# Optimization experiments

Hardware: AMD Instinct MI355X
Metric: run time of the kernel (lower is better)

The kernel has to match this reference:

```python
import jax, jax.numpy as jnp
import numpy as np

B, S, HID = 1, 2048, 1024
H, HKV, D = 16, 4, 64
THETA = 10000.0


def _rope_tables(seq_len, head_dim):
    # Matches RotaryEmbedding: emb = cat(freqs, freqs); kernel reads cos/sin at even
    # positions d for each rotated pair (d, d+1), i.e. columns 0::2 of the table.
    inv_freq = 1.0 / (THETA ** (jnp.arange(0, head_dim, 2, dtype=jnp.float32) / head_dim))
    freqs = jnp.arange(seq_len, dtype=jnp.float32)[:, None] * inv_freq[None, :]  # [S, D/2]
    emb = jnp.concatenate([freqs, freqs], axis=-1)  # [S, D]
    return jnp.cos(emb)[:, 0::2], jnp.sin(emb)[:, 0::2]  # each [S, D/2]


def _apply_rope(x, cos, sin):
    # x: [B, H, S, D]; rotate interleaved pairs (2i, 2i+1) as in the kernel.
    xe, xo = x[..., 0::2], x[..., 1::2]
    re = xe * cos - xo * sin
    ro = xe * sin + xo * cos
    return jnp.stack([re, ro], axis=-1).reshape(x.shape)


def setup_inputs() -> dict:
    key = jax.random.key(0)
    k0, k1, k2, k3, k4 = jax.random.split(key, 5)
    return {
        "hidden_states": jax.random.normal(k0, (B, S, HID), dtype=jnp.float32),
        "Wq": jax.random.normal(k1, (HID, H * D), dtype=jnp.float32) * 0.02,
        "Wk": jax.random.normal(k2, (HID, HKV * D), dtype=jnp.float32) * 0.02,
        "Wv": jax.random.normal(k3, (HID, HKV * D), dtype=jnp.float32) * 0.02,
        "Wo": jax.random.normal(k4, (H * D, HID), dtype=jnp.float32) * 0.02,
    }


def reference(hidden_states, Wq, Wk, Wv, Wo):
    b, s, _ = hidden_states.shape
    q = (hidden_states @ Wq).reshape(b, s, H, D).transpose(0, 2, 1, 3)    # [B,H,S,D]
    k = (hidden_states @ Wk).reshape(b, s, HKV, D).transpose(0, 2, 1, 3)  # [B,Hkv,S,D]
    v = (hidden_states @ Wv).reshape(b, s, HKV, D).transpose(0, 2, 1, 3)

    cos, sin = _rope_tables(s, D)
    q = _apply_rope(q, cos, sin)
    k = _apply_rope(k, cos, sin)

    G = H // HKV  # GQA group size: query head h -> kv head h // G
    qg = q.reshape(b, HKV, G, s, D)
    scale = jnp.float32(D) ** -0.5
    scores = jnp.einsum("bkgqd,bkpd->bkgqp", qg, k) * scale  # [B,Hkv,G,S,S]
    causal = jnp.tril(jnp.ones((s, s), dtype=bool))
    scores = jnp.where(causal, scores, jnp.float32(-1e30))
    probs = jax.nn.softmax(scores, axis=-1)
    out = jnp.einsum("bkgqp,bkpd->bkgqd", probs, v).reshape(b, H, s, D)
    out = out.transpose(0, 2, 1, 3).reshape(b, s, H * D)
    return out @ Wo
```

## Files before the change

kernel.cpp:

```cpp
#include <hip/hip_runtime.h>
#include <hip/hip_bf16.h>
#include <math.h>

#define SEQ   2048
#define HID   1024
#define NH    16
#define NKV   4
#define DH    64
#define GQ    (NH / NKV)
#define NQKV  1536
#define KT    64
#define QB    32
#define CH    512
#define NCH   (SEQ / CH)
#define PSTR  72
#define LNSC  0.2878231366f
#define GS    528
#define BUFS  (8 * GS)

typedef __attribute__((ext_vector_type(8))) short bf16x8;
typedef __attribute__((ext_vector_type(4))) float f32x4;
typedef unsigned short u16;
typedef unsigned int u32;

__device__ __forceinline__ u16 f2bf(float f) {
    union { float f; unsigned u; } x; x.f = f;
    unsigned r = x.u + 0x7fffu + ((x.u >> 16) & 1u);
    return (u16)(r >> 16);
}
__device__ __forceinline__ u32 pk2bf(float lo, float hi) {
    return (u32)f2bf(lo) | ((u32)f2bf(hi) << 16);
}
__device__ __forceinline__ void load_lds16(const u16* g, u16* l) {
    __builtin_amdgcn_global_load_lds(
        (const __attribute__((address_space(1))) unsigned int*)g,
        (__attribute__((address_space(3))) unsigned int*)l, 16, 0, 0);
}

__global__ __launch_bounds__(256) void setup(const float* __restrict__ X,
                                             const float* __restrict__ Wq,
                                             const float* __restrict__ Wk,
                                             const float* __restrict__ Wv,
                                             const float* __restrict__ Wo,
                                             u16* __restrict__ Xb,
                                             u16* __restrict__ Wt,
                                             u16* __restrict__ WoT) {
    const int z = blockIdx.z;
    if (z == 4) {
        const int idx = ((int)blockIdx.y * 64 + (int)blockIdx.x) * 256 + threadIdx.x;
        const float4 v = ((const float4*)X)[idx];
        ushort4 o;
        o.x = f2bf(v.x); o.y = f2bf(v.y); o.z = f2bf(v.z); o.w = f2bf(v.w);
        ((ushort4*)Xb)[idx] = o;
        return;
    }
    const float* in; u16* out; int N;
    if (z == 0)      { in = Wq; out = Wt;                             N = HID; }
    else if (z == 1) { in = Wk; out = Wt + (size_t)HID * HID;         N = 256; }
    else if (z == 2) { in = Wv; out = Wt + (size_t)(HID + 256) * HID; N = 256; }
    else             { in = Wo; out = WoT;                            N = HID; }

    const int n0 = blockIdx.x * 32;
    if (n0 >= N) return;
    const int k0 = blockIdx.y * 32;

    __shared__ float t[32][33];
    const int tx = threadIdx.x & 31;
    const int ty = threadIdx.x >> 5;
    #pragma unroll
    for (int i = 0; i < 4; ++i)
        t[ty + i * 8][tx] = in[(size_t)(k0 + ty + i * 8) * N + n0 + tx];
    __syncthreads();
    #pragma unroll
    for (int i = 0; i < 4; ++i)
        out[(size_t)(n0 + ty + i * 8) * HID + k0 + tx] = f2bf(t[tx][ty + i * 8]);
}

__global__ __launch_bounds__(256) void gemm_qkv(const u16* __restrict__ A,
                                                const u16* __restrict__ Bt,
                                                u16* __restrict__ Qb,
                                                u16* __restrict__ Kb,
                                                u16* __restrict__ VTg) {
    __shared__ u16 Bs[2 * BUFS];

    const int tid  = threadIdx.x;
    const int lane = tid & 63;
    const int w    = tid >> 6;
    const int c    = lane & 15;
    const int quad = lane >> 4;
    const int m0   = blockIdx.y * 64;
    const int n0   = blockIdx.x * 64;

    const u16* gB0 = Bt + (size_t)(n0 + w * 16 + (lane >> 3)) * HID + (lane & 7) * 8;
    const u16* gB1 = gB0 + (size_t)8 * HID;
    const int  gofs0 = (w * 2) * GS, gofs1 = (w * 2 + 1) * GS;

    const u16* gA = A + (size_t)(m0 + w * 16 + c) * HID + quad * 8;
    const int  bfoff = (c >> 3) * GS + (c & 7) * 64 + quad * 8;

    f32x4 acc[4];
    #pragma unroll
    for (int nt = 0; nt < 4; ++nt) acc[nt] = (f32x4){0.f, 0.f, 0.f, 0.f};

    bf16x8 afc[2], afn[2];
    afc[0] = *(const bf16x8*)gA;
    afc[1] = *(const bf16x8*)(gA + 32);
    load_lds16(gB0, &Bs[gofs0]);
    load_lds16(gB1, &Bs[gofs1]);

    const int T = HID / 64;
    for (int t = 0; t < T; ++t) {
        __syncthreads();
        if (t + 1 < T) {
            const int nb = ((t + 1) & 1) * BUFS;
            load_lds16(gB0 + (t + 1) * 64, &Bs[nb + gofs0]);
            load_lds16(gB1 + (t + 1) * 64, &Bs[nb + gofs1]);
            afn[0] = *(const bf16x8*)(gA + (t + 1) * 64);
            afn[1] = *(const bf16x8*)(gA + (t + 1) * 64 + 32);
        }
        const int b = (t & 1) * BUFS;
        bf16x8 bfr[4][2];
        #pragma unroll
        for (int nt = 0; nt < 4; ++nt)
            #pragma unroll
            for (int ks = 0; ks < 2; ++ks)
                bfr[nt][ks] = *(const bf16x8*)&Bs[b + nt * (2 * GS) + ks * 32 + bfoff];
        #pragma unroll
        for (int ks = 0; ks < 2; ++ks)
            #pragma unroll
            for (int nt = 0; nt < 4; ++nt)
                acc[nt] = __builtin_amdgcn_mfma_f32_16x16x32_bf16(afc[ks], bfr[nt][ks], acc[nt], 0, 0, 0);
        afc[0] = afn[0];
        afc[1] = afn[1];
    }

    const int s0 = m0 + w * 16 + quad * 4;
    if (n0 < 1280) {
        const bool isQ = (n0 < 1024);
        #pragma unroll
        for (int nt = 0; nt < 4; ++nt) {
            const int d = nt * 16 + c;
            const float inv_freq = __expf(-(float)(d & 30) * LNSC);
            const float sgn = (d & 1) ? 1.f : -1.f;
            #pragma unroll
            for (int rg = 0; rg < 4; ++rg) {
                const float self = acc[nt][rg];
                const float partner = __shfl_xor(self, 1);
                float sn, cs;
                __sincosf((float)(s0 + rg) * inv_freq, &sn, &cs);
                float o = fmaf(partner, sgn * sn, self * cs);
                if (isQ) {
                    Qb[(size_t)(s0 + rg) * HID + n0 + d] = f2bf(o * 0.125f);
                } else {
                    const int kh = (n0 - 1024) >> 6;
                    Kb[((size_t)kh * SEQ + s0 + rg) * DH + d] = f2bf(o);
                }
            }
        }
    } else {
        const int kh = (n0 - 1280) >> 6;
        #pragma unroll
        for (int nt = 0; nt < 4; ++nt) {
            const int d = nt * 16 + c;
            ushort4 o;
            o.x = f2bf(acc[nt][0]); o.y = f2bf(acc[nt][1]);
            o.z = f2bf(acc[nt][2]); o.w = f2bf(acc[nt][3]);
            *(ushort4*)&VTg[((size_t)kh * DH + d) * SEQ + s0] = o;
        }
    }
}

__global__ __launch_bounds__(256) void gemm64(const u16* __restrict__ A,
                                              const u16* __restrict__ Bt,
                                              float* __restrict__ C,
                                              int K, int ldc) {
    __shared__ u16 Bs[2 * BUFS];

    const int tid  = threadIdx.x;
    const int lane = tid & 63;
    const int w    = tid >> 6;
    const int c    = lane & 15;
    const int quad = lane >> 4;
    const int m0   = blockIdx.y * 64;
    const int n0   = blockIdx.x * 64;

    const u16* gB0 = Bt + (size_t)(n0 + w * 16 + (lane >> 3)) * K + (lane & 7) * 8;
    const u16* gB1 = gB0 + (size_t)8 * K;
    const int  gofs0 = (w * 2) * GS, gofs1 = (w * 2 + 1) * GS;

    const u16* gA = A + (size_t)(m0 + w * 16 + c) * K + quad * 8;
    const int  bfoff = (c >> 3) * GS + (c & 7) * 64 + quad * 8;

    f32x4 acc[4];
    #pragma unroll
    for (int nt = 0; nt < 4; ++nt) acc[nt] = (f32x4){0.f, 0.f, 0.f, 0.f};

    bf16x8 afc[2], afn[2];
    afc[0] = *(const bf16x8*)gA;
    afc[1] = *(const bf16x8*)(gA + 32);
    load_lds16(gB0, &Bs[gofs0]);
    load_lds16(gB1, &Bs[gofs1]);

    const int T = K / 64;
    for (int t = 0; t < T; ++t) {
        __syncthreads();
        if (t + 1 < T) {
            const int nb = ((t + 1) & 1) * BUFS;
            load_lds16(gB0 + (t + 1) * 64, &Bs[nb + gofs0]);
            load_lds16(gB1 + (t + 1) * 64, &Bs[nb + gofs1]);
            afn[0] = *(const bf16x8*)(gA + (t + 1) * 64);
            afn[1] = *(const bf16x8*)(gA + (t + 1) * 64 + 32);
        }
        const int b = (t & 1) * BUFS;
        bf16x8 bfr[4][2];
        #pragma unroll
        for (int nt = 0; nt < 4; ++nt)
            #pragma unroll
            for (int ks = 0; ks < 2; ++ks)
                bfr[nt][ks] = *(const bf16x8*)&Bs[b + nt * (2 * GS) + ks * 32 + bfoff];
        #pragma unroll
        for (int ks = 0; ks < 2; ++ks)
            #pragma unroll
            for (int nt = 0; nt < 4; ++nt)
                acc[nt] = __builtin_amdgcn_mfma_f32_16x16x32_bf16(afc[ks], bfr[nt][ks], acc[nt], 0, 0, 0);
        afc[0] = afn[0];
        afc[1] = afn[1];
    }

    #pragma unroll
    for (int nt = 0; nt < 4; ++nt)
        #pragma unroll
        for (int rg = 0; rg < 4; ++rg)
            C[(size_t)(m0 + w * 16 + quad * 4 + rg) * ldc + n0 + nt * 16 + c] = acc[nt][rg];
}

__global__ __launch_bounds__(256) void attn_kernel(const u16* __restrict__ Qb,
                                                   const u16* __restrict__ Kb,
                                                   const u16* __restrict__ VTg,
                                                   float* __restrict__ Opart,
                                                   float* __restrict__ lpart,
                                                   u16* __restrict__ At) {
    __shared__ u16 Ks[2][2][64 * 32];
    __shared__ u16 Vs[2][2][64 * 32];
    __shared__ u16 Pst[4][QB * PSTR];

    const int tid  = threadIdx.x;
    const int lane = tid & 63;
    const int w    = tid >> 6;
    const int c    = lane & 15;
    const int quad = lane >> 4;
    const int kh   = blockIdx.y;
    const int z    = blockIdx.z;
    const int qt   = (SEQ / QB - 1) - (int)blockIdx.x;
    const int q0   = qt * QB;
    const int h    = kh * GQ + w;

    const int kstart = z * CH;
    const int klim   = q0 + QB;
    if (kstart >= klim) return;
    const int kend   = (klim < kstart + CH) ? klim : (kstart + CH);
    const int ntiles = (kend - kstart + KT - 1) / KT;

    bf16x8 qf[2][2];
    #pragma unroll
    for (int g = 0; g < 2; ++g)
        #pragma unroll
        for (int ks = 0; ks < 2; ++ks)
            qf[g][ks] = *(const bf16x8*)&Qb[(size_t)(q0 + g * 16 + c) * HID + h * DH + ks * 32 + quad * 8];

    f32x4 accO[4][2];
    #pragma unroll
    for (int nt = 0; nt < 4; ++nt)
        #pragma unroll
        for (int g = 0; g < 2; ++g)
            accO[nt][g] = (f32x4){0.f, 0.f, 0.f, 0.f};
    float l[2] = {0.f, 0.f};

    const int hf = w >> 1;
    const int g0 = (w & 1) * 2;
    const int srow = (lane >> 2);
    const int scol = (lane & 3) * 8;

    {
        #pragma unroll
        for (int gi = 0; gi < 2; ++gi) {
            const int g = g0 + gi;
            load_lds16(Kb + ((size_t)kh * SEQ + kstart + g * 16 + srow) * DH + hf * 32 + scol,
                       &Ks[0][hf][(g * 16) * 32]);
            load_lds16(VTg + ((size_t)kh * DH + g * 16 + srow) * SEQ + kstart + hf * 32 + scol,
                       &Vs[0][hf][(g * 16) * 32]);
        }
    }

    for (int t = 0; t < ntiles; ++t) {
        const int kt0 = kstart + t * KT;
        __syncthreads();
        if (t + 1 < ntiles) {
            const int nk = kt0 + KT;
            const int nb = (t + 1) & 1;
            #pragma unroll
            for (int gi = 0; gi < 2; ++gi) {
                const int g = g0 + gi;
                load_lds16(Kb + ((size_t)kh * SEQ + nk + g * 16 + srow) * DH + hf * 32 + scol,
                           &Ks[nb][hf][(g * 16) * 32]);
                load_lds16(VTg + ((size_t)kh * DH + g * 16 + srow) * SEQ + nk + hf * 32 + scol,
                           &Vs[nb][hf][(g * 16) * 32]);
            }
        }
        const int b = t & 1;

        f32x4 accS[4][2];
        #pragma unroll
        for (int nS = 0; nS < 4; ++nS)
            #pragma unroll
            for (int g = 0; g < 2; ++g)
                accS[nS][g] = (f32x4){0.f, 0.f, 0.f, 0.f};
        #pragma unroll
        for (int nS = 0; nS < 4; ++nS)
            #pragma unroll
            for (int ks = 0; ks < 2; ++ks) {
                const bf16x8 kf = *(const bf16x8*)&Ks[b][ks][(nS * 16 + c) * 32 + quad * 8];
                #pragma unroll
                for (int g = 0; g < 2; ++g)
                    accS[nS][g] = __builtin_amdgcn_mfma_f32_16x16x32_bf16(kf, qf[g][ks], accS[nS][g], 0, 0, 0);
            }

        #pragma unroll
        for (int g = 0; g < 2; ++g) {
            const int q = q0 + g * 16 + c;
            #pragma unroll
            for (int nS = 0; nS < 4; ++nS) {
                const int key = kt0 + nS * 16 + quad * 4;
                const float p0 = (key + 0 <= q) ? __expf(accS[nS][g][0]) : 0.f;
                const float p1 = (key + 1 <= q) ? __expf(accS[nS][g][1]) : 0.f;
                const float p2 = (key + 2 <= q) ? __expf(accS[nS][g][2]) : 0.f;
                const float p3 = (key + 3 <= q) ? __expf(accS[nS][g][3]) : 0.f;
                l[g] += (p0 + p1) + (p2 + p3);
                u32* dst = (u32*)&Pst[w][(g * 16 + c) * PSTR + nS * 16 + quad * 4];
                dst[0] = pk2bf(p0, p1);
                dst[1] = pk2bf(p2, p3);
            }
        }
        __threadfence_block();

        #pragma unroll
        for (int ks2 = 0; ks2 < 2; ++ks2) {
            bf16x8 pf[2];
            #pragma unroll
            for (int g = 0; g < 2; ++g)
                pf[g] = *(const bf16x8*)&Pst[w][(g * 16 + c) * PSTR + ks2 * 32 + quad * 8];
            #pragma unroll
            for (int nt = 0; nt < 4; ++nt) {
                const bf16x8 vf = *(const bf16x8*)&Vs[b][ks2][(nt * 16 + c) * 32 + quad * 8];
                #pragma unroll
                for (int g = 0; g < 2; ++g)
                    accO[nt][g] = __builtin_amdgcn_mfma_f32_16x16x32_bf16(vf, pf[g], accO[nt][g], 0, 0, 0);
            }
        }
    }

    const int nchunks = (q0 + QB + CH - 1) / CH;

    if (nchunks == 1) {
        #pragma unroll
        for (int g = 0; g < 2; ++g) {
            float lg = l[g];
            lg += __shfl_xor(lg, 16);
            lg += __shfl_xor(lg, 32);
            const float inv = 1.0f / lg;
            u16* Ap = At + (size_t)(q0 + g * 16 + c) * HID + h * DH;
            #pragma unroll
            for (int nt = 0; nt < 4; ++nt) {
                ushort4 o;
                o.x = f2bf(accO[nt][g][0] * inv);
                o.y = f2bf(accO[nt][g][1] * inv);
                o.z = f2bf(accO[nt][g][2] * inv);
                o.w = f2bf(accO[nt][g][3] * inv);
                *(ushort4*)&Ap[nt * 16 + quad * 4] = o;
            }
        }
        return;
    }

    #pragma unroll
    for (int g = 0; g < 2; ++g) {
        float lg = l[g];
        lg += __shfl_xor(lg, 16);
        lg += __shfl_xor(lg, 32);
        if (quad == 0)
            lpart[((size_t)z * SEQ + q0 + g * 16 + c) * NH + h] = lg;

        float* Op = Opart + ((size_t)z * SEQ + q0 + g * 16 + c) * HID + h * DH;
        #pragma unroll
        for (int nt = 0; nt < 4; ++nt)
            *(f32x4*)&Op[nt * 16 + quad * 4] = accO[nt][g];
    }
}

__global__ __launch_bounds__(256) void attn_reduce(const float* __restrict__ Opart,
                                                   const float* __restrict__ lpart,
                                                   u16* __restrict__ At) {
    const int idx = blockIdx.x * 256 + threadIdx.x + (CH * HID / 4);
    const int q  = idx >> 8;
    const int h  = (idx & 255) >> 4;
    const int klim = (q & ~(QB - 1)) + QB;
    float4 o = ((const float4*)Opart)[idx];
    float  l = lpart[q * NH + h];
    #pragma unroll
    for (int z = 1; z < NCH; ++z) {
        if (z * CH < klim) {
            const float4 o1 = ((const float4*)Opart)[idx + z * (SEQ * HID / 4)];
            o.x += o1.x; o.y += o1.y; o.z += o1.z; o.w += o1.w;
            l += lpart[(z * SEQ + q) * NH + h];
        }
    }
    const float inv = 1.0f / l;
    ushort4 r;
    r.x = f2bf(o.x * inv); r.y = f2bf(o.y * inv);
    r.z = f2bf(o.z * inv); r.w = f2bf(o.w * inv);
    ((ushort4*)At)[idx] = r;
}

extern "C" void kernel_launch(void* const* d_in, const int* in_sizes, int n_in,
                              void* d_out, int out_size, void* d_ws, size_t ws_size,
                              hipStream_t stream) {
    const float* X  = (const float*)d_in[0];
    const float* Wq = (const float*)d_in[1];
    const float* Wk = (const float*)d_in[2];
    const float* Wv = (const float*)d_in[3];
    const float* Wo = (const float*)d_in[4];
    float* out = (float*)d_out;

    u16* Wt     = (u16*)d_ws;
    u16* WoT    = Wt + (size_t)NQKV * HID;
    u16* Xb     = WoT + (size_t)HID * HID;
    u16* At     = Xb + (size_t)SEQ * HID;
    u16* Qb     = At + (size_t)SEQ * HID;
    u16* Kb     = Qb + (size_t)SEQ * HID;
    u16* VTg    = Kb + (size_t)NKV * SEQ * DH;
    float* Opart = (float*)(VTg + (size_t)NKV * DH * SEQ);
    float* lpart = Opart + (size_t)NCH * SEQ * HID;

    dim3 blk(256);

    setup<<<dim3(64, 32, 5), blk, 0, stream>>>(X, Wq, Wk, Wv, Wo, Xb, Wt, WoT);

    gemm_qkv<<<dim3(NQKV / 64, SEQ / 64), blk, 0, stream>>>(Xb, Wt, Qb, Kb, VTg);

    attn_kernel<<<dim3(SEQ / QB, NKV, NCH), blk, 0, stream>>>(Qb, Kb, VTg, Opart, lpart, At);

    attn_reduce<<<((SEQ - CH) * HID / 4) / 256, blk, 0, stream>>>(Opart, lpart, At);

    gemm64<<<dim3(HID / 64, SEQ / 64), blk, 0, stream>>>(At, WoT, out, HID, HID);
}
```

Before: 136.4 us.

## Swizzle K/V LDS tiles, use exp2 with folded log2e, skip masking on full tiles

K and V tiles move from a split half-column LDS layout to full 64-wide rows with an XOR swizzle, applied both to the global-to-LDS load addresses and to the MFMA fragment reads, to avoid bank conflicts. The Q scale now folds in log2(e), so the softmax uses the hardware exp2 instruction instead of __expf. Tiles that lie fully below the causal diagonal skip the per-element mask compares. The software bf16 rounding is replaced by the packed v_cvt_pk_bf16_f32 instruction, whose rounding may differ slightly.

```diff
diff --git a/kernel.cpp b/kernel.cpp
--- a/kernel.cpp
+++ b/kernel.cpp
@@ -17,6 +17,7 @@
 #define LNSC  0.2878231366f
 #define GS    528
 #define BUFS  (8 * GS)
+#define QSCALE 0.18033688011112042f
 
 typedef __attribute__((ext_vector_type(8))) short bf16x8;
 typedef __attribute__((ext_vector_type(4))) float f32x4;
@@ -28,8 +29,10 @@
     unsigned r = x.u + 0x7fffu + ((x.u >> 16) & 1u);
     return (u16)(r >> 16);
 }
-__device__ __forceinline__ u32 pk2bf(float lo, float hi) {
-    return (u32)f2bf(lo) | ((u32)f2bf(hi) << 16);
+__device__ __forceinline__ u32 cvtpk(float lo, float hi) {
+    u32 r;
+    asm("v_cvt_pk_bf16_f32 %0, %1, %2" : "=v"(r) : "v"(lo), "v"(hi));
+    return r;
 }
 __device__ __forceinline__ void load_lds16(const u16* g, u16* l) {
     __builtin_amdgcn_global_load_lds(
@@ -150,7 +153,7 @@
                 __sincosf((float)(s0 + rg) * inv_freq, &sn, &cs);
                 float o = fmaf(partner, sgn * sn, self * cs);
                 if (isQ) {
-                    Qb[(size_t)(s0 + rg) * HID + n0 + d] = f2bf(o * 0.125f);
+                    Qb[(size_t)(s0 + rg) * HID + n0 + d] = f2bf(o * QSCALE);
                 } else {
                     const int kh = (n0 - 1024) >> 6;
                     Kb[((size_t)kh * SEQ + s0 + rg) * DH + d] = f2bf(o);
@@ -240,8 +243,8 @@
                                                    float* __restrict__ Opart,
                                                    float* __restrict__ lpart,
                                                    u16* __restrict__ At) {
-    __shared__ u16 Ks[2][2][64 * 32];
-    __shared__ u16 Vs[2][2][64 * 32];
+    __shared__ u16 Ks[2][64 * 64];
+    __shared__ u16 Vs[2][64 * 64];
     __shared__ u16 Pst[4][QB * PSTR];
 
     const int tid  = threadIdx.x;
@@ -276,20 +279,16 @@
             accO[nt][g] = (f32x4){0.f, 0.f, 0.f, 0.f};
     float l[2] = {0.f, 0.f};
 
-    const int hf = w >> 1;
-    const int g0 = (w & 1) * 2;
-    const int srow = (lane >> 2);
-    const int scol = (lane & 3) * 8;
-
-    {
-        #pragma unroll
-        for (int gi = 0; gi < 2; ++gi) {
-            const int g = g0 + gi;
-            load_lds16(Kb + ((size_t)kh * SEQ + kstart + g * 16 + srow) * DH + hf * 32 + scol,
-                       &Ks[0][hf][(g * 16) * 32]);
-            load_lds16(VTg + ((size_t)kh * DH + g * 16 + srow) * SEQ + kstart + hf * 32 + scol,
-                       &Vs[0][hf][(g * 16) * 32]);
-        }
+    const int rr = lane >> 3;
+    const int sw = ((lane & 7) ^ rr) * 8;
+
+    #pragma unroll
+    for (int gi = 0; gi < 2; ++gi) {
+        const int row = w * 16 + gi * 8;
+        load_lds16(Kb + ((size_t)kh * SEQ + kstart + row + rr) * DH + sw,
+                   &Ks[0][row * 64]);
+        load_lds16(VTg + ((size_t)kh * DH + row + rr) * SEQ + kstart + sw,
+                   &Vs[0][row * 64]);
     }
 
     for (int t = 0; t < ntiles; ++t) {
@@ -300,11 +299,11 @@
             const int nb = (t + 1) & 1;
             #pragma unroll
             for (int gi = 0; gi < 2; ++gi) {
-                const int g = g0 + gi;
-                load_lds16(Kb + ((size_t)kh * SEQ + nk + g * 16 + srow) * DH + hf * 32 + scol,
-                           &Ks[nb][hf][(g * 16) * 32]);
-                load_lds16(VTg + ((size_t)kh * DH + g * 16 + srow) * SEQ + nk + hf * 32 + scol,
-                           &Vs[nb][hf][(g * 16) * 32]);
+                const int row = w * 16 + gi * 8;
+                load_lds16(Kb + ((size_t)kh * SEQ + nk + row + rr) * DH + sw,
+                           &Ks[nb][row * 64]);
+                load_lds16(VTg + ((size_t)kh * DH + row + rr) * SEQ + nk + sw,
+                           &Vs[nb][row * 64]);
             }
         }
         const int b = t & 1;
@@ -319,7 +318,8 @@
         for (int nS = 0; nS < 4; ++nS)
             #pragma unroll
             for (int ks = 0; ks < 2; ++ks) {
-                const bf16x8 kf = *(const bf16x8*)&Ks[b][ks][(nS * 16 + c) * 32 + quad * 8];
+                const bf16x8 kf = *(const bf16x8*)
+                    &Ks[b][(nS * 16 + c) * 64 + (((ks * 4 + quad) ^ (c & 7)) * 8)];
                 #pragma unroll
                 for (int g = 0; g < 2; ++g)
                     accS[nS][g] = __builtin_amdgcn_mfma_f32_16x16x32_bf16(kf, qf[g][ks], accS[nS][g], 0, 0, 0);
@@ -328,17 +328,26 @@
         #pragma unroll
         for (int g = 0; g < 2; ++g) {
             const int q = q0 + g * 16 + c;
+            const bool full = (kt0 + KT - 1 <= q0 + g * 16);
             #pragma unroll
             for (int nS = 0; nS < 4; ++nS) {
                 const int key = kt0 + nS * 16 + quad * 4;
-                const float p0 = (key + 0 <= q) ? __expf(accS[nS][g][0]) : 0.f;
-                const float p1 = (key + 1 <= q) ? __expf(accS[nS][g][1]) : 0.f;
-                const float p2 = (key + 2 <= q) ? __expf(accS[nS][g][2]) : 0.f;
-                const float p3 = (key + 3 <= q) ? __expf(accS[nS][g][3]) : 0.f;
+                float p0, p1, p2, p3;
+                if (full) {
+                    p0 = __builtin_amdgcn_exp2f(accS[nS][g][0]);
+                    p1 = __builtin_amdgcn_exp2f(accS[nS][g][1]);
+                    p2 = __builtin_amdgcn_exp2f(accS[nS][g][2]);
+                    p3 = __builtin_amdgcn_exp2f(accS[nS][g][3]);
+                } else {
+                    p0 = (key + 0 <= q) ? __builtin_amdgcn_exp2f(accS[nS][g][0]) : 0.f;
+                    p1 = (key + 1 <= q) ? __builtin_amdgcn_exp2f(accS[nS][g][1]) : 0.f;
+                    p2 = (key + 2 <= q) ? __builtin_amdgcn_exp2f(accS[nS][g][2]) : 0.f;
+                    p3 = (key + 3 <= q) ? __builtin_amdgcn_exp2f(accS[nS][g][3]) : 0.f;
+                }
                 l[g] += (p0 + p1) + (p2 + p3);
                 u32* dst = (u32*)&Pst[w][(g * 16 + c) * PSTR + nS * 16 + quad * 4];
-                dst[0] = pk2bf(p0, p1);
-                dst[1] = pk2bf(p2, p3);
+                dst[0] = cvtpk(p0, p1);
+                dst[1] = cvtpk(p2, p3);
             }
         }
         __threadfence_block();
@@ -351,7 +360,8 @@
                 pf[g] = *(const bf16x8*)&Pst[w][(g * 16 + c) * PSTR + ks2 * 32 + quad * 8];
             #pragma unroll
             for (int nt = 0; nt < 4; ++nt) {
-                const bf16x8 vf = *(const bf16x8*)&Vs[b][ks2][(nt * 16 + c) * 32 + quad * 8];
+                const bf16x8 vf = *(const bf16x8*)
+                    &Vs[b][(nt * 16 + c) * 64 + (((ks2 * 4 + quad) ^ (c & 7)) * 8)];
                 #pragma unroll
                 for (int g = 0; g < 2; ++g)
                     accO[nt][g] = __builtin_amdgcn_mfma_f32_16x16x32_bf16(vf, pf[g], accO[nt][g], 0, 0, 0);
```

Result: faster. 131.4 us (-3.7%).
